# Optimization experiments

Hardware: AMD Instinct MI355X
Metric: run time of the kernel (lower is better)

## Reference

```python
import jax, jax.numpy as jnp
from jax import lax
import numpy as np

EPS = 1e-8
B, SA, SB = 32, 64, 64
H, WD, L, V, CLS = 128, 300, 20, 50000, 3


def _div(n, d):
    # faithful to div_with_small_value: clamp denominator at EPS
    return n / jnp.where(d > EPS, d, EPS)


def _lstm(x, Wih, Whh, bih, bhh):
    # PyTorch gate order: i, f, g, o. x: [B, S, D] -> outputs [B, S, H], last h [B, H]
    def step(carry, xt):
        h, c = carry
        g = xt @ Wih.T + bih + h @ Whh.T + bhh
        i, f, gg, o = jnp.split(g, 4, axis=-1)
        c = jax.nn.sigmoid(f) * c + jax.nn.sigmoid(i) * jnp.tanh(gg)
        h = jax.nn.sigmoid(o) * jnp.tanh(c)
        return (h, c), h
    h0 = jnp.zeros((x.shape[0], Whh.shape[1]), x.dtype)
    (hT, _), hs = lax.scan(step, (h0, h0), jnp.swapaxes(x, 0, 1))
    return jnp.swapaxes(hs, 0, 1), hT


def _bilstm(x, pf, pb):
    of, _ = _lstm(x, *pf)
    ob, _ = _lstm(x[:, ::-1], *pb)
    return jnp.concatenate([of, ob[:, ::-1]], axis=-1)


def _full_match(v1, v2, w):
    # v1: [B,S,H]; v2: [B,H] or [B,S,H]; w: [L,H] -> [B,S,L]
    v1p = v1[:, :, None, :] * w
    v2p = (v2[:, None, None, :] if v2.ndim == 2 else v2[:, :, None, :]) * w
    num = jnp.sum(v1p * v2p, -1)
    den = jnp.linalg.norm(v1p, axis=-1) * jnp.linalg.norm(v2p, axis=-1)
    return _div(num, den)


def _maxpool_match(v1, v2, w):
    # cosine between every (i, j) pair under each perspective -> [B,SA,SB,L]
    v1p = v1[:, :, None, :] * w  # [B,SA,L,H]
    v2p = v2[:, :, None, :] * w  # [B,SB,L,H]
    num = jnp.einsum('bild,bjld->bijl', v1p, v2p)
    den = jnp.linalg.norm(v1p, axis=-1)[:, :, None, :] * jnp.linalg.norm(v2p, axis=-1)[:, None, :, :]
    return _div(num, den)


def _attention(v1, v2):
    # cosine similarity matrix [B,SA,SB]
    num = jnp.einsum('bid,bjd->bij', v1, v2)
    den = jnp.linalg.norm(v1, axis=-1)[:, :, None] * jnp.linalg.norm(v2, axis=-1)[:, None, :]
    return _div(num, den)


def setup_inputs():
    key = jax.random.key(0)
    ks = iter(jax.random.split(key, 64))
    def nrm(shape, s=0.05):
        return jax.random.normal(next(ks), shape, jnp.float32) * s
    inp = {
        'Atoken': jax.random.randint(next(ks), (B, SA), 0, V),
        'Btoken': jax.random.randint(next(ks), (B, SB), 0, V),
        'word_emb': nrm((V, WD), 0.1),
    }
    for d in ('f', 'b'):
        inp['ctx_Wih_' + d] = nrm((4 * H, WD))
        inp['ctx_Whh_' + d] = nrm((4 * H, H))
        inp['ctx_bih_' + d] = jnp.zeros(4 * H, jnp.float32)
        inp['ctx_bhh_' + d] = jnp.zeros(4 * H, jnp.float32)
        inp['agg_Wih_' + d] = nrm((4 * H, 8 * L))
        inp['agg_Whh_' + d] = nrm((4 * H, H))
        inp['agg_bih_' + d] = jnp.zeros(4 * H, jnp.float32)
        inp['agg_bhh_' + d] = jnp.zeros(4 * H, jnp.float32)
    for i in range(1, 9):
        inp['mp_w%d' % i] = nrm((L, H), 0.1)
    inp['fc1_W'] = nrm((2 * H, 4 * H))
    inp['fc1_b'] = jnp.zeros(2 * H, jnp.float32)
    inp['fc2_W'] = nrm((CLS, 2 * H))
    inp['fc2_b'] = jnp.zeros(CLS, jnp.float32)
    return inp


def reference(Atoken, Btoken, word_emb,
              ctx_Wih_f, ctx_Whh_f, ctx_bih_f, ctx_bhh_f,
              ctx_Wih_b, ctx_Whh_b, ctx_bih_b, ctx_bhh_b,
              mp_w1, mp_w2, mp_w3, mp_w4, mp_w5, mp_w6, mp_w7, mp_w8,
              agg_Wih_f, agg_Whh_f, agg_bih_f, agg_bhh_f,
              agg_Wih_b, agg_Whh_b, agg_bih_b, agg_bhh_b,
              fc1_W, fc1_b, fc2_W, fc2_b):
    A = word_emb[Atoken]   # [B,SA,WD]
    Bx = word_emb[Btoken]  # [B,SB,WD]
    pf = (ctx_Wih_f, ctx_Whh_f, ctx_bih_f, ctx_bhh_f)
    pb = (ctx_Wih_b, ctx_Whh_b, ctx_bih_b, ctx_bhh_b)
    cA = _bilstm(A, pf, pb)
    cB = _bilstm(Bx, pf, pb)
    cA_f, cA_b = cA[..., :H], cA[..., H:]
    cB_f, cB_b = cB[..., :H], cB[..., H:]

    # full matching against last fw / first bw states
    mvA_full_f = _full_match(cA_f, cB_f[:, -1], mp_w1)
    mvA_full_b = _full_match(cA_b, cB_b[:, 0], mp_w2)
    mvB_full_f = _full_match(cB_f, cA_f[:, -1], mp_w1)
    mvB_full_b = _full_match(cB_b, cA_b[:, 0], mp_w2)

    # max-pooling matching
    mm_f = _maxpool_match(cA_f, cB_f, mp_w3)  # [B,SA,SB,L]
    mm_b = _maxpool_match(cA_b, cB_b, mp_w4)
    mvA_max_f = mm_f.max(2); mvA_max_b = mm_b.max(2)
    mvB_max_f = mm_f.max(1); mvB_max_b = mm_b.max(1)

    # attentive matching
    att_f = _attention(cA_f, cB_f)  # [B,SA,SB]
    att_b = _attention(cA_b, cB_b)
    mean_B_f = _div(jnp.einsum('bij,bjd->bid', att_f, cB_f), att_f.sum(2, keepdims=True))
    mean_B_b = _div(jnp.einsum('bij,bjd->bid', att_b, cB_b), att_b.sum(2, keepdims=True))
    mean_A_f = _div(jnp.einsum('bij,bid->bjd', att_f, cA_f), att_f.sum(1)[:, :, None])
    mean_A_b = _div(jnp.einsum('bij,bid->bjd', att_b, cA_b), att_b.sum(1)[:, :, None])
    mvA_am_f = _full_match(cA_f, mean_B_f, mp_w5)
    mvA_am_b = _full_match(cA_b, mean_B_b, mp_w6)
    mvB_am_f = _full_match(cB_f, mean_A_f, mp_w5)
    mvB_am_b = _full_match(cB_b, mean_A_b, mp_w6)

    # attentive-max matching (broadcast-multiply-reduce, the headroom hotspot)
    max_B_f = jnp.max(cB_f[:, None, :, :] * att_f[..., None], axis=2)  # [B,SA,H]
    max_B_b = jnp.max(cB_b[:, None, :, :] * att_b[..., None], axis=2)
    max_A_f = jnp.max(cA_f[:, :, None, :] * att_f[..., None], axis=1)  # [B,SB,H]
    max_A_b = jnp.max(cA_b[:, :, None, :] * att_b[..., None], axis=1)
    mvA_ax_f = _full_match(cA_f, max_B_f, mp_w7)
    mvA_ax_b = _full_match(cA_b, max_B_b, mp_w8)
    mvB_ax_f = _full_match(cB_f, max_A_f, mp_w7)
    mvB_ax_b = _full_match(cB_b, max_A_b, mp_w8)

    mvA = jnp.concatenate([mvA_full_f, mvA_max_f, mvA_am_f, mvA_ax_f,
                           mvA_full_b, mvA_max_b, mvA_am_b, mvA_ax_b], axis=2)  # [B,SA,8L]
    mvB = jnp.concatenate([mvB_full_f, mvB_max_f, mvB_am_f, mvB_ax_f,
                           mvB_full_b, mvB_max_b, mvB_am_b, mvB_ax_b], axis=2)

    apf = (agg_Wih_f, agg_Whh_f, agg_bih_f, agg_bhh_f)
    apb = (agg_Wih_b, agg_Whh_b, agg_bih_b, agg_bhh_b)
    _, hAf = _lstm(mvA, *apf); _, hAb = _lstm(mvA[:, ::-1], *apb)
    _, hBf = _lstm(mvB, *apf); _, hBb = _lstm(mvB[:, ::-1], *apb)
    out = jnp.concatenate([hAf, hAb, hBf, hBb], axis=1)  # [B, 4H]
    out = jnp.tanh(out @ fc1_W.T + fc1_b)
    logits = out @ fc2_W.T + fc2_b
    return jax.nn.softmax(logits, axis=-1)
```

## Files before the change

### kernel.cpp

```cpp
#include <hip/hip_runtime.h>
#include <math.h>


#define EPSV 1e-8f

__device__ __forceinline__ float sigm(float x) { return 1.f / (1.f + __expf(-x)); }
__device__ __forceinline__ float tanh_f(float x) {
    float t = expm1f(-2.f * fabsf(x));
    float r = -t / (t + 2.f);
    return copysignf(r, x);
}
__device__ __forceinline__ float divg(float n, float d) { return n / (d > EPSV ? d : EPSV); }

template<bool GATHER>
__global__ __launch_bounds__(256)
void gemm_gin(const float* __restrict__ X,
              const int* __restrict__ tokA, const int* __restrict__ tokB,
              const float* __restrict__ emb,
              const float* __restrict__ Wf, const float* __restrict__ Wb,
              const float* __restrict__ bihF, const float* __restrict__ bhhF,
              const float* __restrict__ bihB, const float* __restrict__ bhhB,
              int K, float* __restrict__ Gout)
{
    const int tid = threadIdx.x;
    const int tx = tid & 15, ty = tid >> 4;
    const int m0 = blockIdx.x * 64;
    const int n0 = blockIdx.y * 64;
    const int dir = (n0 >= 512) ? 1 : 0;
    const float* Wd = dir ? Wb : Wf;
    const int nn0 = n0 & 511;

    __shared__ __align__(16) float As[16][64];
    __shared__ __align__(16) float Bs[16][64];

    const int sm = tid & 63;
    const int sq = tid >> 6;
    const int kq_off = sq << 2;

    const float* arow;
    if (GATHER) {
        const int mg = m0 + sm;
        const int tok = (mg < 2048) ? tokA[mg] : tokB[mg - 2048];
        arow = emb + (size_t)tok * 300;
    } else {
        arow = X + (size_t)(m0 + sm) * K;
    }
    const float* brow = Wd + (size_t)(nn0 + sm) * K;

    float acc[4][4];
#pragma unroll
    for (int r = 0; r < 4; ++r)
#pragma unroll
        for (int c = 0; c < 4; ++c) acc[r][c] = 0.f;

    float4 av = make_float4(0.f, 0.f, 0.f, 0.f);
    float4 bv = make_float4(0.f, 0.f, 0.f, 0.f);
    {
        const int kq = kq_off;
        if (kq + 4 <= K) {
            av = *(const float4*)(arow + kq);
            bv = *(const float4*)(brow + kq);
        }
    }

    for (int k0 = 0; k0 < K; k0 += 16) {
        __syncthreads();
        As[kq_off + 0][sm] = av.x;
        As[kq_off + 1][sm] = av.y;
        As[kq_off + 2][sm] = av.z;
        As[kq_off + 3][sm] = av.w;
        Bs[kq_off + 0][sm] = bv.x;
        Bs[kq_off + 1][sm] = bv.y;
        Bs[kq_off + 2][sm] = bv.z;
        Bs[kq_off + 3][sm] = bv.w;
        __syncthreads();

        av = make_float4(0.f, 0.f, 0.f, 0.f);
        bv = make_float4(0.f, 0.f, 0.f, 0.f);
        const int kq = k0 + 16 + kq_off;
        if (kq + 4 <= K) {
            av = *(const float4*)(arow + kq);
            bv = *(const float4*)(brow + kq);
        }

#pragma unroll
        for (int k = 0; k < 16; ++k) {
            float4 a = *(const float4*)(&As[k][ty << 2]);
            float4 b = *(const float4*)(&Bs[k][tx << 2]);
            acc[0][0] += a.x * b.x; acc[0][1] += a.x * b.y; acc[0][2] += a.x * b.z; acc[0][3] += a.x * b.w;
            acc[1][0] += a.y * b.x; acc[1][1] += a.y * b.y; acc[1][2] += a.y * b.z; acc[1][3] += a.y * b.w;
            acc[2][0] += a.z * b.x; acc[2][1] += a.z * b.y; acc[2][2] += a.z * b.z; acc[2][3] += a.z * b.w;
            acc[3][0] += a.w * b.x; acc[3][1] += a.w * b.y; acc[3][2] += a.w * b.z; acc[3][3] += a.w * b.w;
        }
    }

    const float* bih = dir ? bihB : bihF;
    const float* bhh = dir ? bhhB : bhhF;
    const int chain = ((m0 >= 2048) ? 2 : 0) + dir;
    const int nn = nn0 + (tx << 2);
    float b0 = bih[nn] + bhh[nn];
    float b1 = bih[nn + 1] + bhh[nn + 1];
    float b2 = bih[nn + 2] + bhh[nn + 2];
    float b3 = bih[nn + 3] + bhh[nn + 3];
#pragma unroll
    for (int r = 0; r < 4; ++r) {
        int m = m0 + (ty << 2) + r;
        int row = m & 2047;
        float4 o;
        o.x = acc[r][0] + b0; o.y = acc[r][1] + b1; o.z = acc[r][2] + b2; o.w = acc[r][3] + b3;
        *(float4*)(Gout + ((size_t)chain * 2048 + row) * 512 + nn) = o;
    }
}

__global__ __launch_bounds__(512, 2)
void lstm_kernel(const float* __restrict__ Gin,
                 const float* __restrict__ WhhF, const float* __restrict__ WhhB,
                 float* __restrict__ outH, float* __restrict__ hfin, int storeAll)
{
    const int tid = threadIdx.x;
    const int chain = blockIdx.x >> 5;
    const int b = blockIdx.x & 31;
    const int rev = chain & 1;
    const float* Whh = rev ? WhhB : WhhF;

    __shared__ float4 hs4[32];
    __shared__ float gact[512];
    float* hs = (float*)hs4;

    float4 w4[32];
    const float4* wrow = (const float4*)(Whh + (size_t)tid * 128);
#pragma unroll
    for (int q = 0; q < 32; ++q) w4[q] = wrow[q];

    if (tid < 32) hs4[tid] = make_float4(0.f, 0.f, 0.f, 0.f);
    float c_reg = 0.f;
    __syncthreads();

    const size_t base = ((size_t)chain * 32 + b) * 64;
    float gin_cur = Gin[(base + (rev ? 63 : 0)) * 512 + tid];

    for (int t = 0; t < 64; ++t) {
        const int s_cur = rev ? 63 - t : t;
        float gin_next = 0.f;
        if (t + 1 < 64) {
            int s_next = rev ? 62 - t : t + 1;
            gin_next = Gin[(base + s_next) * 512 + tid];
        }
        float a0 = 0.f, a1 = 0.f, a2 = 0.f, a3 = 0.f;
#pragma unroll
        for (int q = 0; q < 32; ++q) {
            float4 h4 = hs4[q];
            a0 += h4.x * w4[q].x; a1 += h4.y * w4[q].y;
            a2 += h4.z * w4[q].z; a3 += h4.w * w4[q].w;
        }
        float g = gin_cur + ((a0 + a1) + (a2 + a3));
        gact[tid] = ((tid >> 7) == 2) ? tanh_f(g) : sigm(g);
        __syncthreads();
        if (tid < 128) {
            float iv = gact[tid], fv = gact[128 + tid], gv = gact[256 + tid], ov = gact[384 + tid];
            c_reg = fv * c_reg + iv * gv;
            float hv = ov * tanh_f(c_reg);
            hs[tid] = hv;
            if (storeAll) outH[(base + s_cur) * 128 + tid] = hv;
        }
        __syncthreads();
        gin_cur = gin_next;
    }
    if (!storeAll && tid < 128) hfin[(size_t)b * 512 + chain * 128 + tid] = hs[tid];
}

__global__ __launch_bounds__(256)
void attn_kernel(const float* __restrict__ ctxH, float* __restrict__ att)
{
    const int tid = threadIdx.x;
    const int b = blockIdx.x;
    const int dir = blockIdx.y;
    const float* cA = ctxH + (((size_t)dir * 32 + b) * 64) * 128;
    const float* cB = ctxH + (((size_t)(2 + dir) * 32 + b) * 64) * 128;
    __shared__ __align__(16) float sa[64 * 132];
    __shared__ __align__(16) float sb[64 * 132];
    __shared__ float na[64], nb[64];

    for (int e = tid; e < 8192; e += 256) {
        int i = e >> 7, k = e & 127;
        sa[i * 132 + k] = cA[e];
        sb[i * 132 + k] = cB[e];
    }
    __syncthreads();
    if (tid < 64) {
        float s = 0.f;
        for (int k = 0; k < 128; ++k) { float v = sa[tid * 132 + k]; s += v * v; }
        na[tid] = sqrtf(s);
    } else if (tid < 128) {
        int j = tid - 64; float s = 0.f;
        for (int k = 0; k < 128; ++k) { float v = sb[j * 132 + k]; s += v * v; }
        nb[j] = sqrtf(s);
    }
    __syncthreads();

    const int tx = tid & 15, ty = tid >> 4;
    float acc[4][4] = {};
    for (int k4 = 0; k4 < 32; ++k4) {
        float4 av[4], bv[4];
#pragma unroll
        for (int r = 0; r < 4; ++r) av[r] = *(const float4*)(sa + ((ty << 2) + r) * 132 + (k4 << 2));
#pragma unroll
        for (int c = 0; c < 4; ++c) bv[c] = *(const float4*)(sb + ((tx << 2) + c) * 132 + (k4 << 2));
#pragma unroll
        for (int r = 0; r < 4; ++r)
#pragma unroll
            for (int c = 0; c < 4; ++c)
                acc[r][c] += av[r].x * bv[c].x + av[r].y * bv[c].y + av[r].z * bv[c].z + av[r].w * bv[c].w;
    }
    float* attb = att + (((size_t)dir * 32 + b) * 64) * 64;
#pragma unroll
    for (int r = 0; r < 4; ++r) {
        int i = (ty << 2) + r;
#pragma unroll
        for (int c = 0; c < 4; ++c) {
            int j = (tx << 2) + c;
            attb[i * 64 + j] = divg(acc[r][c], na[i] * nb[j]);
        }
    }
}

__global__ __launch_bounds__(256)
void meanmax_kernel(const float* __restrict__ ctxH, const float* __restrict__ att,
                    float* __restrict__ meanB, float* __restrict__ meanA,
                    float* __restrict__ maxB, float* __restrict__ maxA)
{
    const int tid = threadIdx.x;
    const int b = blockIdx.x, dir = blockIdx.y, side = blockIdx.z;
    __shared__ float sat[64 * 68];
    __shared__ __align__(16) float sc[64 * 132];
    __shared__ float ssum[64];

    const float* attb = att + (((size_t)dir * 32 + b) * 64) * 64;
    const int chain_src = side ? dir : (2 + dir);
    const float* cS = ctxH + (((size_t)chain_src * 32 + b) * 64) * 128;

    for (int e = tid; e < 4096; e += 256) sat[(e >> 6) * 68 + (e & 63)] = attb[e];
    for (int e = tid; e < 8192; e += 256) sc[(e >> 7) * 132 + (e & 127)] = cS[e];
    __syncthreads();
    if (tid < 64) {
        float s = 0.f;
        for (int q = 0; q < 64; ++q) s += side ? sat[q * 68 + tid] : sat[tid * 68 + q];
        ssum[tid] = s;
    }
    __syncthreads();

    const int r = tid >> 2;
    const int d0 = (tid & 3) * 32;
    float4 am[8], axv[8];
#pragma unroll
    for (int p = 0; p < 8; ++p) {
        am[p] = make_float4(0.f, 0.f, 0.f, 0.f);
        axv[p] = make_float4(-INFINITY, -INFINITY, -INFINITY, -INFINITY);
    }
    for (int q = 0; q < 64; ++q) {
        float a = side ? sat[q * 68 + r] : sat[r * 68 + q];
#pragma unroll
        for (int p = 0; p < 8; ++p) {
            float4 cv = *(const float4*)(sc + q * 132 + d0 + (p << 2));
            float px = a * cv.x, py = a * cv.y, pz = a * cv.z, pw = a * cv.w;
            am[p].x += px; am[p].y += py; am[p].z += pz; am[p].w += pw;
            axv[p].x = fmaxf(axv[p].x, px); axv[p].y = fmaxf(axv[p].y, py);
            axv[p].z = fmaxf(axv[p].z, pz); axv[p].w = fmaxf(axv[p].w, pw);
        }
    }
    float den = ssum[r] > EPSV ? ssum[r] : EPSV;
    float inv = 1.f / den;
    float* mout = (side ? meanA : meanB) + (((size_t)dir * 32 + b) * 64 + r) * 128 + d0;
    float* xout = (side ? maxA : maxB) + (((size_t)dir * 32 + b) * 64 + r) * 128 + d0;
#pragma unroll
    for (int p = 0; p < 8; ++p) {
        float4 o;
        o.x = am[p].x * inv; o.y = am[p].y * inv; o.z = am[p].z * inv; o.w = am[p].w * inv;
        *(float4*)(mout + (p << 2)) = o;
        *(float4*)(xout + (p << 2)) = axv[p];
    }
}

__global__ __launch_bounds__(256)
void mm_kernel(const float* __restrict__ ctxH,
               const float* __restrict__ mpw3, const float* __restrict__ mpw4,
               float* __restrict__ mvA, float* __restrict__ mvB)
{
    const int tid = threadIdx.x;
    const int b = blockIdx.x, l = blockIdx.y, dir = blockIdx.z;
    const float* wsrc = (dir ? mpw4 : mpw3) + (size_t)l * 128;
    __shared__ float wl[128];
    __shared__ __align__(16) float su[64 * 132];
    __shared__ __align__(16) float sv[64 * 132];
    __shared__ float nu[64], nv[64];
    __shared__ float smm[64 * 68];

    const float* cA = ctxH + (((size_t)dir * 32 + b) * 64) * 128;
    const float* cB = ctxH + (((size_t)(2 + dir) * 32 + b) * 64) * 128;

    if (tid < 128) wl[tid] = wsrc[tid];
    __syncthreads();
    for (int e = tid; e < 8192; e += 256) {
        int i = e >> 7, k = e & 127;
        float w = wl[k];
        su[i * 132 + k] = cA[e] * w;
        sv[i * 132 + k] = cB[e] * w;
    }
    __syncthreads();
    if (tid < 64) {
        float s = 0.f;
        for (int k = 0; k < 128; ++k) { float v = su[tid * 132 + k]; s += v * v; }
        nu[tid] = sqrtf(s);
    } else if (tid < 128) {
        int j = tid - 64; float s = 0.f;
        for (int k = 0; k < 128; ++k) { float v = sv[j * 132 + k]; s += v * v; }
        nv[j] = sqrtf(s);
    }
    __syncthreads();

    const int tx = tid & 15, ty = tid >> 4;
    float acc[4][4] = {};
    for (int k4 = 0; k4 < 32; ++k4) {
        float4 av[4], bv[4];
#pragma unroll
        for (int r = 0; r < 4; ++r) av[r] = *(const float4*)(su + ((ty << 2) + r) * 132 + (k4 << 2));
#pragma unroll
        for (int c = 0; c < 4; ++c) bv[c] = *(const float4*)(sv + ((tx << 2) + c) * 132 + (k4 << 2));
#pragma unroll
        for (int r = 0; r < 4; ++r)
#pragma unroll
            for (int c = 0; c < 4; ++c)
                acc[r][c] += av[r].x * bv[c].x + av[r].y * bv[c].y + av[r].z * bv[c].z + av[r].w * bv[c].w;
    }
#pragma unroll
    for (int r = 0; r < 4; ++r) {
        int i = (ty << 2) + r;
#pragma unroll
        for (int c = 0; c < 4; ++c) {
            int j = (tx << 2) + c;
            smm[i * 68 + j] = divg(acc[r][c], nu[i] * nv[j]);
        }
    }
    __syncthreads();
    const int blkoff = (dir ? 5 : 1) * 20 + l;
    if (tid < 64) {
        float mx = -INFINITY;
        for (int j = 0; j < 64; ++j) mx = fmaxf(mx, smm[tid * 68 + j]);
        mvA[((size_t)b * 64 + tid) * 160 + blkoff] = mx;
    } else if (tid < 128) {
        int j = tid - 64;
        float mx = -INFINITY;
        for (int i = 0; i < 64; ++i) mx = fmaxf(mx, smm[i * 68 + j]);
        mvB[((size_t)b * 64 + j) * 160 + blkoff] = mx;
    }
}

__global__ __launch_bounds__(256)
void fm_kernel(const float* __restrict__ ctxH,
               const float* __restrict__ meanB, const float* __restrict__ meanA,
               const float* __restrict__ maxB, const float* __restrict__ maxA,
               const float* __restrict__ w1, const float* __restrict__ w2,
               const float* __restrict__ w5, const float* __restrict__ w6,
               const float* __restrict__ w7, const float* __restrict__ w8,
               float* __restrict__ mvA, float* __restrict__ mvB)
{
    const int tid = threadIdx.x;
    const int b = blockIdx.x, dir = blockIdx.y, side = blockIdx.z;
    __shared__ __align__(16) float sc[64 * 132];
    __shared__ __align__(16) float st[64 * 132];
    __shared__ __align__(16) float sw[20 * 132];

    const int chain_self = side ? (2 + dir) : dir;
    const float* cX = ctxH + (((size_t)chain_self * 32 + b) * 64) * 128;
    for (int e = tid; e < 8192; e += 256) sc[(e >> 7) * 132 + (e & 127)] = cX[e];

    for (int kind = 0; kind < 3; ++kind) {
        const float* w = (kind == 0) ? (dir ? w2 : w1)
                       : (kind == 1) ? (dir ? w6 : w5)
                                     : (dir ? w8 : w7);
        __syncthreads();
        if (kind == 0) {
            const int chain_o = side ? dir : (2 + dir);
            const float* trow = ctxH + (((size_t)chain_o * 32 + b) * 64 + (dir ? 0 : 63)) * 128;
            for (int e = tid; e < 128; e += 256) st[e] = trow[e];
        } else {
            const float* tsrc = (kind == 1) ? (side ? meanA : meanB) : (side ? maxA : maxB);
            tsrc += (((size_t)dir * 32 + b) * 64) * 128;
            for (int e = tid; e < 8192; e += 256) st[(e >> 7) * 132 + (e & 127)] = tsrc[e];
        }
        for (int e = tid; e < 2560; e += 256) sw[(e >> 7) * 132 + (e & 127)] = w[e];
        __syncthreads();

        const int blk = ((kind == 0) ? 0 : (kind == 1) ? 2 : 3) + (dir ? 4 : 0);
        float* mv = side ? mvB : mvA;
        for (int o = tid; o < 1280; o += 256) {
            int i = o / 20;
            int l = o - i * 20;
            const float* crow = sc + i * 132;
            const float* trow = st + ((kind == 0) ? 0 : i * 132);
            const float* wrow = sw + l * 132;
            float num = 0.f, na = 0.f, nb = 0.f;
#pragma unroll 8
            for (int k4 = 0; k4 < 32; ++k4) {
                float4 a = *(const float4*)(crow + (k4 << 2));
                float4 t = *(const float4*)(trow + (k4 << 2));
                float4 wv = *(const float4*)(wrow + (k4 << 2));
                float ax = a.x * wv.x, ay = a.y * wv.y, az = a.z * wv.z, aw = a.w * wv.w;
                float tx_ = t.x * wv.x, ty_ = t.y * wv.y, tz_ = t.z * wv.z, tw_ = t.w * wv.w;
                num += ax * tx_ + ay * ty_ + az * tz_ + aw * tw_;
                na  += ax * ax  + ay * ay  + az * az  + aw * aw;
                nb  += tx_ * tx_ + ty_ * ty_ + tz_ * tz_ + tw_ * tw_;
            }
            float den = sqrtf(na) * sqrtf(nb);
            mv[((size_t)b * 64 + i) * 160 + blk * 20 + l] = divg(num, den);
        }
    }
}

__global__ __launch_bounds__(256)
void head_kernel(const float* __restrict__ hfin,
                 const float* __restrict__ fc1W, const float* __restrict__ fc1b,
                 const float* __restrict__ fc2W, const float* __restrict__ fc2b,
                 float* __restrict__ out)
{
    const int b = blockIdx.x, tid = threadIdx.x;
    __shared__ __align__(16) float sx[512];
    __shared__ float sy[256], sl[3];
    for (int e = tid; e < 512; e += 256) sx[e] = hfin[(size_t)b * 512 + e];
    __syncthreads();
    {
        float acc = fc1b[tid];
        const float4* wr = (const float4*)(fc1W + (size_t)tid * 512);
#pragma unroll 8
        for (int k4 = 0; k4 < 128; ++k4) {
            float4 w = wr[k4];
            float4 x = *(const float4*)(sx + (k4 << 2));
            acc += w.x * x.x + w.y * x.y + w.z * x.z + w.w * x.w;
        }
        sy[tid] = tanh_f(acc);
    }
    __syncthreads();
    if (tid < 3) {
        float acc = fc2b[tid];
        for (int n = 0; n < 256; ++n) acc += sy[n] * fc2W[tid * 256 + n];
        sl[tid] = acc;
    }
    __syncthreads();
    if (tid < 3) {
        float m = fmaxf(sl[0], fmaxf(sl[1], sl[2]));
        float e0 = expf(sl[0] - m), e1 = expf(sl[1] - m), e2 = expf(sl[2] - m);
        float s = e0 + e1 + e2;
        float v = (tid == 0) ? e0 : ((tid == 1) ? e1 : e2);
        out[b * 3 + tid] = v / s;
    }
}

extern "C" void kernel_launch(void* const* d_in, const int* in_sizes, int n_in,
                              void* d_out, int out_size, void* d_ws, size_t ws_size,
                              hipStream_t stream)
{
    const bool dictOrder = (n_in > 7 && in_sizes[7] == 81920);
    int iCtxWih[2], iCtxWhh[2], iCtxBih[2], iCtxBhh[2];
    int iAggWih[2], iAggWhh[2], iAggBih[2], iAggBhh[2];
    int iW[8], iFc1W, iFc1b, iFc2W, iFc2b;
    if (dictOrder) {
        iCtxWih[0] = 3;  iCtxWhh[0] = 4;  iCtxBih[0] = 5;  iCtxBhh[0] = 6;
        iAggWih[0] = 7;  iAggWhh[0] = 8;  iAggBih[0] = 9;  iAggBhh[0] = 10;
        iCtxWih[1] = 11; iCtxWhh[1] = 12; iCtxBih[1] = 13; iCtxBhh[1] = 14;
        iAggWih[1] = 15; iAggWhh[1] = 16; iAggBih[1] = 17; iAggBhh[1] = 18;
        for (int k = 0; k < 8; ++k) iW[k] = 19 + k;
        iFc1W = 27; iFc1b = 28; iFc2W = 29; iFc2b = 30;
    } else {
        iCtxWih[0] = 3;  iCtxWhh[0] = 4;  iCtxBih[0] = 5;  iCtxBhh[0] = 6;
        iCtxWih[1] = 7;  iCtxWhh[1] = 8;  iCtxBih[1] = 9;  iCtxBhh[1] = 10;
        for (int k = 0; k < 8; ++k) iW[k] = 11 + k;
        iAggWih[0] = 19; iAggWhh[0] = 20; iAggBih[0] = 21; iAggBhh[0] = 22;
        iAggWih[1] = 23; iAggWhh[1] = 24; iAggBih[1] = 25; iAggBhh[1] = 26;
        iFc1W = 27; iFc1b = 28; iFc2W = 29; iFc2b = 30;
    }

    const int*   tokA = (const int*)d_in[0];
    const int*   tokB = (const int*)d_in[1];
    const float* emb  = (const float*)d_in[2];
    const float* ctxWihF = (const float*)d_in[iCtxWih[0]];
    const float* ctxWihB = (const float*)d_in[iCtxWih[1]];
    const float* ctxWhhF = (const float*)d_in[iCtxWhh[0]];
    const float* ctxWhhB = (const float*)d_in[iCtxWhh[1]];
    const float* ctxBihF = (const float*)d_in[iCtxBih[0]];
    const float* ctxBihB = (const float*)d_in[iCtxBih[1]];
    const float* ctxBhhF = (const float*)d_in[iCtxBhh[0]];
    const float* ctxBhhB = (const float*)d_in[iCtxBhh[1]];
    const float* aggWihF = (const float*)d_in[iAggWih[0]];
    const float* aggWihB = (const float*)d_in[iAggWih[1]];
    const float* aggWhhF = (const float*)d_in[iAggWhh[0]];
    const float* aggWhhB = (const float*)d_in[iAggWhh[1]];
    const float* aggBihF = (const float*)d_in[iAggBih[0]];
    const float* aggBihB = (const float*)d_in[iAggBih[1]];
    const float* aggBhhF = (const float*)d_in[iAggBhh[0]];
    const float* aggBhhB = (const float*)d_in[iAggBhh[1]];
    const float* mw[8];
    for (int k = 0; k < 8; ++k) mw[k] = (const float*)d_in[iW[k]];
    const float* fc1W = (const float*)d_in[iFc1W];
    const float* fc1b = (const float*)d_in[iFc1b];
    const float* fc2W = (const float*)d_in[iFc2W];
    const float* fc2b = (const float*)d_in[iFc2b];

    float* Wp    = (float*)d_ws;
    float* Gin   = Wp;
    float* ctxH  = Gin + 4194304;
    float* attw  = ctxH + 1048576;
    float* meanB = attw + 262144;
    float* meanA = meanB + 524288;
    float* maxB  = meanA + 524288;
    float* maxA  = maxB + 524288;
    float* mv    = maxA + 524288;
    float* hfin  = mv + 655360;
    float* mvA   = mv;
    float* mvB   = mv + (size_t)2048 * 160;

    dim3 gGemm(64, 16);

    gemm_gin<true><<<gGemm, 256, 0, stream>>>(
        nullptr, tokA, tokB, emb, ctxWihF, ctxWihB,
        ctxBihF, ctxBhhF, ctxBihB, ctxBhhB, 300, Gin);

    lstm_kernel<<<128, 512, 0, stream>>>(Gin, ctxWhhF, ctxWhhB, ctxH, hfin, 1);

    attn_kernel<<<dim3(32, 2), 256, 0, stream>>>(ctxH, attw);

    meanmax_kernel<<<dim3(32, 2, 2), 256, 0, stream>>>(ctxH, attw, meanB, meanA, maxB, maxA);

    mm_kernel<<<dim3(32, 20, 2), 256, 0, stream>>>(ctxH, mw[2], mw[3], mvA, mvB);

    fm_kernel<<<dim3(32, 2, 2), 256, 0, stream>>>(ctxH, meanB, meanA, maxB, maxA,
        mw[0], mw[1], mw[4], mw[5], mw[6], mw[7], mvA, mvB);

    gemm_gin<false><<<gGemm, 256, 0, stream>>>(
        mv, nullptr, nullptr, nullptr, aggWihF, aggWihB,
        aggBihF, aggBhhF, aggBihB, aggBhhB, 160, Gin);

    lstm_kernel<<<128, 512, 0, stream>>>(Gin, aggWhhF, aggWhhB, ctxH, hfin, 0);

    head_kernel<<<32, 256, 0, stream>>>(hfin, fc1W, fc1b, fc2W, fc2b, (float*)d_out);

    (void)out_size; (void)ws_size;
}
```

Before: 490.1 us.

## Split LSTM recurrent dot product across two thread halves with 1024-thread blocks

The LSTM recurrence kernel now uses 1024 threads per block. Each gate row's 128-element dot product is split into two 64-element halves whose partial sums go to separate shared arrays, so the serial per-step FMA chain is halved and each thread holds half as many weight registers. Gate activations move to the 128 cell-update threads, which sum both partials before applying sigmoid or tanh. tanh is also reimplemented with a clamped __expf instead of expm1f; this is cheaper but slightly less accurate near zero.

```diff
diff --git a/kernel.cpp b/kernel.cpp
--- a/kernel.cpp
+++ b/kernel.cpp
@@ -6,8 +6,9 @@
 
 __device__ __forceinline__ float sigm(float x) { return 1.f / (1.f + __expf(-x)); }
 __device__ __forceinline__ float tanh_f(float x) {
-    float t = expm1f(-2.f * fabsf(x));
-    float r = -t / (t + 2.f);
+    float ax = fminf(fabsf(x), 20.f);
+    float e = __expf(2.f * ax);
+    float r = (e - 1.f) / (e + 1.f);
     return copysignf(r, x);
 }
 __device__ __forceinline__ float divg(float n, float d) { return n / (d > EPSV ? d : EPSV); }
@@ -112,52 +113,62 @@
     }
 }
 
-__global__ __launch_bounds__(512, 2)
+__global__ __launch_bounds__(1024, 4)
 void lstm_kernel(const float* __restrict__ Gin,
                  const float* __restrict__ WhhF, const float* __restrict__ WhhB,
                  float* __restrict__ outH, float* __restrict__ hfin, int storeAll)
 {
     const int tid = threadIdx.x;
+    const int g = tid & 511;
+    const int kh = tid >> 9;
     const int chain = blockIdx.x >> 5;
     const int b = blockIdx.x & 31;
     const int rev = chain & 1;
     const float* Whh = rev ? WhhB : WhhF;
 
     __shared__ float4 hs4[32];
-    __shared__ float gact[512];
+    __shared__ float pl[512];
+    __shared__ float ph[512];
     float* hs = (float*)hs4;
 
-    float4 w4[32];
-    const float4* wrow = (const float4*)(Whh + (size_t)tid * 128);
-#pragma unroll
-    for (int q = 0; q < 32; ++q) w4[q] = wrow[q];
-
-    if (tid < 32) hs4[tid] = make_float4(0.f, 0.f, 0.f, 0.f);
+    float4 w4[16];
+    const float4* wrow = (const float4*)(Whh + (size_t)g * 128 + kh * 64);
+#pragma unroll
+    for (int q = 0; q < 16; ++q) w4[q] = wrow[q];
+
+    if (tid < 128) hs[tid] = 0.f;
     float c_reg = 0.f;
     __syncthreads();
 
     const size_t base = ((size_t)chain * 32 + b) * 64;
-    float gin_cur = Gin[(base + (rev ? 63 : 0)) * 512 + tid];
-
+    float gin_cur = 0.f;
+    if (kh == 0) gin_cur = Gin[(base + (rev ? 63 : 0)) * 512 + g];
+
+    const int qoff = kh << 4;
     for (int t = 0; t < 64; ++t) {
         const int s_cur = rev ? 63 - t : t;
         float gin_next = 0.f;
-        if (t + 1 < 64) {
+        if (kh == 0 && t + 1 < 64) {
             int s_next = rev ? 62 - t : t + 1;
-            gin_next = Gin[(base + s_next) * 512 + tid];
+            gin_next = Gin[(base + s_next) * 512 + g];
         }
         float a0 = 0.f, a1 = 0.f, a2 = 0.f, a3 = 0.f;
 #pragma unroll
-        for (int q = 0; q < 32; ++q) {
-            float4 h4 = hs4[q];
-            a0 += h4.x * w4[q].x; a1 += h4.y * w4[q].y;
-            a2 += h4.z * w4[q].z; a3 += h4.w * w4[q].w;
-        }
-        float g = gin_cur + ((a0 + a1) + (a2 + a3));
-        gact[tid] = ((tid >> 7) == 2) ? tanh_f(g) : sigm(g);
+        for (int q = 0; q < 16; ++q) {
+            float4 h4 = hs4[qoff + q];
+            float4 w = w4[q];
+            a0 += h4.x * w.x; a1 += h4.y * w.y;
+            a2 += h4.z * w.z; a3 += h4.w * w.w;
+        }
+        float a = (a0 + a1) + (a2 + a3);
+        if (kh == 0) pl[g] = gin_cur + a; else ph[g] = a;
         __syncthreads();
         if (tid < 128) {
-            float iv = gact[tid], fv = gact[128 + tid], gv = gact[256 + tid], ov = gact[384 + tid];
+            float gi = pl[tid]       + ph[tid];
+            float gf = pl[128 + tid] + ph[128 + tid];
+            float gg = pl[256 + tid] + ph[256 + tid];
+            float go = pl[384 + tid] + ph[384 + tid];
+            float iv = sigm(gi), fv = sigm(gf), gv = tanh_f(gg), ov = sigm(go);
             c_reg = fv * c_reg + iv * gv;
             float hv = ov * tanh_f(c_reg);
             hs[tid] = hv;
@@ -524,7 +535,7 @@
         nullptr, tokA, tokB, emb, ctxWihF, ctxWihB,
         ctxBihF, ctxBhhF, ctxBihB, ctxBhhB, 300, Gin);
 
-    lstm_kernel<<<128, 512, 0, stream>>>(Gin, ctxWhhF, ctxWhhB, ctxH, hfin, 1);
+    lstm_kernel<<<128, 1024, 0, stream>>>(Gin, ctxWhhF, ctxWhhB, ctxH, hfin, 1);
 
     attn_kernel<<<dim3(32, 2), 256, 0, stream>>>(ctxH, attw);
 
@@ -539,7 +550,7 @@
         mv, nullptr, nullptr, nullptr, aggWihF, aggWihB,
         aggBihF, aggBhhF, aggBihB, aggBhhB, 160, Gin);
 
-    lstm_kernel<<<128, 512, 0, stream>>>(Gin, aggWhhF, aggWhhB, ctxH, hfin, 0);
+    lstm_kernel<<<128, 1024, 0, stream>>>(Gin, aggWhhF, aggWhhB, ctxH, hfin, 0);
 
     head_kernel<<<32, 256, 0, stream>>>(hfin, fc1W, fc1b, fc2W, fc2b, (float*)d_out);
 
```

New measurement: 480.9 us. Within noise of the previous version (-1.9%).
